# Kernel tuning notes

Hardware: AMD Instinct MI355X
Metric: run time of the kernel (lower is better)

The kernel has to match this reference:

```python
import math
import jax, jax.numpy as jnp
import numpy as np

N = 8192
D_IN = 512
D_E = 512


def setup_inputs() -> dict:
    key = jax.random.key(0)
    k1, k2, k3, k4 = jax.random.split(key, 4)
    x = jax.random.normal(k1, (N, D_IN), dtype=jnp.float32)
    A = jax.random.uniform(k2, (N, N), dtype=jnp.float32)
    # xavier-uniform-ish scaling for the two projection weights
    lim_qkv = math.sqrt(6.0 / (D_IN + 3 * D_E))
    Wqkv = jax.random.uniform(k3, (D_IN, 3 * D_E), dtype=jnp.float32, minval=-lim_qkv, maxval=lim_qkv)
    bqkv = jnp.zeros((3 * D_E,), dtype=jnp.float32)
    lim_o = math.sqrt(6.0 / (D_E + D_E))
    Wo = jax.random.uniform(k4, (D_E, D_E), dtype=jnp.float32, minval=-lim_o, maxval=lim_o)
    bo = jnp.zeros((D_E,), dtype=jnp.float32)
    return {"x": x, "A": A, "Wqkv": Wqkv, "bqkv": bqkv, "Wo": Wo, "bo": bo}


def reference(x, A, Wqkv, bqkv, Wo, bo):
    # qkv projection: [N, 3*D_E]
    qkv = x @ Wqkv + bqkv
    q, k, v = jnp.split(qkv, 3, axis=-1)  # each [N, D_E]
    # graph-adjacency transform of keys
    k = A @ k  # [N, D_E]
    scale = 1.0 / math.sqrt(q.shape[-1])
    attn_logits = (q @ k.T) * scale  # [N, N]
    attention = jax.nn.softmax(attn_logits, axis=-1)
    values = attention @ v  # [N, D_E]
    o = values @ Wo + bo
    return (o, attention)
```

## Files before the change

### kernel.cpp

```cpp
#include <hip/hip_runtime.h>

typedef _Float16 half8 __attribute__((ext_vector_type(8)));
typedef _Float16 half4 __attribute__((ext_vector_type(4)));
typedef float f32x4 __attribute__((ext_vector_type(4)));

__global__ __launch_bounds__(256) void transpose_f32(
    const float* __restrict__ in, int lda,
    float* __restrict__ out, int ldo)
{
  __shared__ float t[32][33];
  const int tx = threadIdx.x & 31, ty = threadIdx.x >> 5;
  const int bc = blockIdx.x * 32, br = blockIdx.y * 32;
#pragma unroll
  for (int i = 0; i < 4; ++i)
    t[ty + 8 * i][tx] = in[(size_t)(br + ty + 8 * i) * lda + bc + tx];
  __syncthreads();
#pragma unroll
  for (int i = 0; i < 4; ++i)
    out[(size_t)(bc + ty + 8 * i) * ldo + br + tx] = t[tx][ty + 8 * i];
}

__global__ __launch_bounds__(256) void transpose_f32_f16(
    const float* __restrict__ in, int lda,
    _Float16* __restrict__ out, int ldo)
{
  __shared__ float t[32][33];
  const int tx = threadIdx.x & 31, ty = threadIdx.x >> 5;
  const int bc = blockIdx.x * 32, br = blockIdx.y * 32;
#pragma unroll
  for (int i = 0; i < 4; ++i)
    t[ty + 8 * i][tx] = in[(size_t)(br + ty + 8 * i) * lda + bc + tx];
  __syncthreads();
#pragma unroll
  for (int i = 0; i < 4; ++i)
    out[(size_t)(bc + ty + 8 * i) * ldo + br + tx] = (_Float16)t[tx][ty + 8 * i];
}

__global__ __launch_bounds__(256) void transpose_f16(
    const _Float16* __restrict__ in, int lda,
    _Float16* __restrict__ out, int ldo)
{
  __shared__ _Float16 t[64][66];
  const int tx = threadIdx.x & 63, ty = threadIdx.x >> 6;
  const int bc = blockIdx.x * 64, br = blockIdx.y * 64;
#pragma unroll
  for (int i = 0; i < 16; ++i)
    t[ty + 4 * i][tx] = in[(size_t)(br + ty + 4 * i) * lda + bc + tx];
  __syncthreads();
#pragma unroll
  for (int i = 0; i < 16; ++i)
    out[(size_t)(bc + ty + 4 * i) * ldo + br + tx] = t[tx][ty + 4 * i];
}

__global__ __launch_bounds__(256) void conv_f32_f16(
    const float4* __restrict__ in, _Float16* __restrict__ out)
{
  size_t i = (size_t)blockIdx.x * 256 + threadIdx.x;
  float4 v = in[i];
  half4 h;
  h[0] = (_Float16)v.x; h[1] = (_Float16)v.y;
  h[2] = (_Float16)v.z; h[3] = (_Float16)v.w;
  ((half4*)out)[i] = h;
}

__global__ __launch_bounds__(256) void halfcolsum16(
    const _Float16* __restrict__ k0T16, float* __restrict__ csum)
{
  const int d = blockIdx.x, tid = threadIdx.x;
  float s = 0.f;
#pragma unroll
  for (int i = 0; i < 4; ++i) {
    half8 h = *(const half8*)(k0T16 + (size_t)d * 8192 + i * 2048 + tid * 8);
#pragma unroll
    for (int j = 0; j < 8; ++j) s += (float)h[j];
  }
#pragma unroll
  for (int off = 32; off; off >>= 1) s += __shfl_xor(s, off);
  __shared__ float r[4];
  if ((tid & 63) == 0) r[tid >> 6] = s;
  __syncthreads();
  if (tid == 0) csum[d] = 0.5f * ((r[0] + r[1]) + (r[2] + r[3]));
}

template<int ASPL,int BSPL,int BM,int BN,int WAVES_M,int WAVES_N,int THREADS,
         int APART,bool KSPLIT,int CMODE,int MINW,int AMODE,int BMODE>
__global__ __launch_bounds__(THREADS, MINW) void gemm_bt(
    const void* __restrict__ Agv, int lda, size_t a_plane,
    const void* __restrict__ Bgv, int ldb, size_t b_plane,
    float* __restrict__ Cg, int ldc, size_t c_plane,
    const float* __restrict__ bias, int K, float scale,
    _Float16* __restrict__ c16out)
{
  constexpr int BK = 32;
  constexpr int WM = BM / WAVES_M, WN = BN / WAVES_N;
  constexpr int FM = WM / 16, FN = WN / 16;
  constexpr int NCA = (BM * 4) / THREADS;
  constexpr int NCB = (BN * 4) / THREADS;
  static_assert((BM * 4) % THREADS == 0 && (BN * 4) % THREADS == 0, "mismatch");
  static_assert(AMODE != 3 || ASPL == 1, "AMODE 3 needs ASPL 1");

  __shared__ _Float16 ldsA[2][ASPL][BM][BK];
  __shared__ _Float16 ldsB[2][BSPL][BN][BK];

  const float*    Ag   = (const float*)Agv;
  const _Float16* Ag16 = (const _Float16*)Agv;
  const float*    Bg   = (const float*)Bgv;
  const _Float16* Bg16 = (const _Float16*)Bgv;

  const int tid  = threadIdx.x;
  const int lane = tid & 63;
  const int wid  = tid >> 6;
  const int wrow = wid / WAVES_N, wcol = wid % WAVES_N;
  const int l15  = lane & 15, g = lane >> 4;
  const int brow = blockIdx.y * BM;
  const int bcol = blockIdx.x * BN;

  if constexpr (KSPLIT) {
    const int kc = blockIdx.z;
    Ag += (size_t)kc * K;  Ag16 += (size_t)kc * K;
    Bg += (size_t)kc * K;  Bg16 += (size_t)kc * K;
    Cg += (size_t)kc * c_plane;
  }

  f32x4 acc[FM][FN];
#pragma unroll
  for (int mi = 0; mi < FM; ++mi)
#pragma unroll
    for (int ni = 0; ni < FN; ++ni)
      acc[mi][ni] = (f32x4){0.f, 0.f, 0.f, 0.f};

  float4 ra[NCA][2], rb[NCB][2];
  half8  rah[NCA], rbh[NCB];

  auto loadAB = [&](int kt) {
    const int k0 = kt * BK;
#pragma unroll
    for (int i = 0; i < NCA; ++i) {
      int c = tid + THREADS * i;
      int row = c >> 2, ci = c & 3;
      if constexpr (AMODE == 3) {
        rah[i] = *(const half8*)(Ag16 + (size_t)(brow + row) * lda + k0 + ci * 8);
      } else if constexpr (AMODE == 1) {
        float4 u0 = make_float4(0.f, 0.f, 0.f, 0.f);
        float4 u1 = make_float4(0.f, 0.f, 0.f, 0.f);
        const _Float16* bp = Ag16 + (size_t)(brow + row) * lda + k0 + ci * 8;
#pragma unroll
        for (int p = 0; p < APART; ++p) {
          half8 hv = *(const half8*)(bp + (size_t)p * a_plane);
          u0.x += (float)hv[0]; u0.y += (float)hv[1]; u0.z += (float)hv[2]; u0.w += (float)hv[3];
          u1.x += (float)hv[4]; u1.y += (float)hv[5]; u1.z += (float)hv[6]; u1.w += (float)hv[7];
        }
        ra[i][0] = u0; ra[i][1] = u1;
      } else {
        const float* bp = Ag + (size_t)(brow + row) * lda + k0 + ci * 8;
        float4 u0 = ((const float4*)bp)[0];
        float4 u1 = ((const float4*)bp)[1];
#pragma unroll
        for (int p = 1; p < APART; ++p) {
          const float* pp = bp + (size_t)p * a_plane;
          float4 w0 = ((const float4*)pp)[0], w1 = ((const float4*)pp)[1];
          u0.x += w0.x; u0.y += w0.y; u0.z += w0.z; u0.w += w0.w;
          u1.x += w1.x; u1.y += w1.y; u1.z += w1.z; u1.w += w1.w;
        }
        ra[i][0] = u0; ra[i][1] = u1;
      }
    }
#pragma unroll
    for (int i = 0; i < NCB; ++i) {
      int c = tid + THREADS * i;
      int row = c >> 2, ci = c & 3;
      if constexpr (BMODE == 3) {
        rbh[i] = *(const half8*)(Bg16 + (size_t)(bcol + row) * ldb + k0 + ci * 8);
      } else {
        const float4* p = (const float4*)(Bg + (size_t)(bcol + row) * ldb + k0 + ci * 8);
        rb[i][0] = p[0]; rb[i][1] = p[1];
      }
    }
  };

  auto stageLDS = [&](int b) {
#pragma unroll
    for (int i = 0; i < NCA; ++i) {
      int c = tid + THREADS * i;
      int row = c >> 2, ci = c & 3;
      int off = row * BK + ((ci ^ ((row >> 1) & 3)) << 3);
      if constexpr (AMODE == 3) {
        *(half8*)(&ldsA[b][0][0][0] + off) = rah[i];
      } else {
        float f[8] = {ra[i][0].x, ra[i][0].y, ra[i][0].z, ra[i][0].w,
                      ra[i][1].x, ra[i][1].y, ra[i][1].z, ra[i][1].w};
        half8 h, l;
#pragma unroll
        for (int j = 0; j < 8; ++j) {
          _Float16 hv = (_Float16)f[j];
          h[j] = hv;
          if (ASPL == 2) l[j] = (_Float16)(f[j] - (float)hv);
        }
        *(half8*)(&ldsA[b][0][0][0] + off) = h;
        if (ASPL == 2) *(half8*)(&ldsA[b][1][0][0] + off) = l;
      }
    }
#pragma unroll
    for (int i = 0; i < NCB; ++i) {
      int c = tid + THREADS * i;
      int row = c >> 2, ci = c & 3;
      int off = row * BK + ((ci ^ ((row >> 1) & 3)) << 3);
      if constexpr (BMODE == 3) {
        *(half8*)(&ldsB[b][0][0][0] + off) = rbh[i];
      } else {
        float f[8] = {rb[i][0].x, rb[i][0].y, rb[i][0].z, rb[i][0].w,
                      rb[i][1].x, rb[i][1].y, rb[i][1].z, rb[i][1].w};
        half8 h, l;
#pragma unroll
        for (int j = 0; j < 8; ++j) {
          _Float16 hv = (_Float16)f[j];
          h[j] = hv;
          if (BSPL == 2) l[j] = (_Float16)(f[j] - (float)hv);
        }
        *(half8*)(&ldsB[b][0][0][0] + off) = h;
        if (BSPL == 2) *(half8*)(&ldsB[b][1][0][0] + off) = l;
      }
    }
  };

  const int nk = K / BK;
  loadAB(0);
  stageLDS(0);
  if (nk > 1) loadAB(1);
  __syncthreads();

  for (int kt = 0; kt < nk; ++kt) {
    const int cur = kt & 1, nxt = cur ^ 1;
    if (kt + 1 < nk) stageLDS(nxt);
    if (kt + 2 < nk) loadAB(kt + 2);

    half8 af[FM][ASPL];
#pragma unroll
    for (int mi = 0; mi < FM; ++mi)
#pragma unroll
      for (int sa = 0; sa < ASPL; ++sa) {
        int row = wrow * WM + mi * 16 + l15;
        af[mi][sa] = *(const half8*)(&ldsA[cur][sa][0][0] + row * BK + ((g ^ ((row >> 1) & 3)) << 3));
      }
#pragma unroll
    for (int ni = 0; ni < FN; ++ni) {
      half8 bf[BSPL];
#pragma unroll
      for (int sb = 0; sb < BSPL; ++sb) {
        int row = wcol * WN + ni * 16 + l15;
        bf[sb] = *(const half8*)(&ldsB[cur][sb][0][0] + row * BK + ((g ^ ((row >> 1) & 3)) << 3));
      }
#pragma unroll
      for (int mi = 0; mi < FM; ++mi)
#pragma unroll
        for (int sa = 0; sa < ASPL; ++sa)
#pragma unroll
          for (int sb = 0; sb < BSPL; ++sb) {
            if (ASPL == 2 && BSPL == 2 && sa == 1 && sb == 1) continue;
            acc[mi][ni] = __builtin_amdgcn_mfma_f32_16x16x32_f16(af[mi][sa], bf[sb], acc[mi][ni], 0, 0, 0);
          }
    }
    __syncthreads();
  }

#pragma unroll
  for (int mi = 0; mi < FM; ++mi)
#pragma unroll
    for (int ni = 0; ni < FN; ++ni) {
      int col = bcol + wcol * WN + ni * 16 + l15;
      float bv = bias ? bias[col] : 0.f;
#pragma unroll
      for (int j = 0; j < 4; ++j) {
        int r = brow + wrow * WM + mi * 16 + g * 4 + j;
        float v = acc[mi][ni][j] * scale + bv;
        if constexpr (CMODE == 2) {
          c16out[(size_t)r * ldc + col] = (_Float16)v;
        } else {
          Cg[(size_t)r * ldc + col] = v;
        }
      }
    }
}

template<int BM,int BN,int THREADS,bool STATS,int MINW>
__global__ __launch_bounds__(THREADS, MINW) void gemm_ff16(
    const _Float16* __restrict__ Ag, int lda,
    const _Float16* __restrict__ Bg, int ldb,
    float* __restrict__ Cg, int ldc,
    int K, float scale,
    float* __restrict__ mxout, float* __restrict__ smout, int ntiles)
{
  constexpr int BK = 32;
  constexpr int WAVES_M = 2, WAVES_N = 2;
  constexpr int WM = BM / WAVES_M, WN = BN / WAVES_N;
  constexpr int FM = WM / 16, FN = WN / 16;
  constexpr int NCA = (BM * 4) / THREADS;
  constexpr int NCB = (BN * 4) / THREADS;

  __shared__ _Float16 ldsA[2][BM][BK];
  __shared__ _Float16 ldsB[2][BN][BK];

  const int tid  = threadIdx.x;
  const int lane = tid & 63;
  const int wid  = tid >> 6;
  const int wrow = wid >> 1, wcol = wid & 1;
  const int l15  = lane & 15, g = lane >> 4;

  const int id = blockIdx.x;
  const int wgid = (id & 7) * 512 + (id >> 3);
  const int bxv = wgid & 63, byv = wgid >> 6;
  const int brow = byv * BM;
  const int bcol = bxv * BN;

  f32x4 acc[FM][FN];
#pragma unroll
  for (int mi = 0; mi < FM; ++mi)
#pragma unroll
    for (int ni = 0; ni < FN; ++ni)
      acc[mi][ni] = (f32x4){0.f, 0.f, 0.f, 0.f};

  half8 ra[NCA], rb[NCB];

  auto loadAB = [&](int kt) {
    const int k0 = kt * BK;
#pragma unroll
    for (int i = 0; i < NCA; ++i) {
      int c = tid + THREADS * i;
      int row = c >> 2, ci = c & 3;
      ra[i] = *(const half8*)(Ag + (size_t)(brow + row) * lda + k0 + ci * 8);
    }
#pragma unroll
    for (int i = 0; i < NCB; ++i) {
      int c = tid + THREADS * i;
      int row = c >> 2, ci = c & 3;
      rb[i] = *(const half8*)(Bg + (size_t)(bcol + row) * ldb + k0 + ci * 8);
    }
  };

  auto stageLDS = [&](int b) {
#pragma unroll
    for (int i = 0; i < NCA; ++i) {
      int c = tid + THREADS * i;
      int row = c >> 2, ci = c & 3;
      int off = row * BK + ((ci ^ ((row >> 1) & 3)) << 3);
      *(half8*)(&ldsA[b][0][0] + off) = ra[i];
    }
#pragma unroll
    for (int i = 0; i < NCB; ++i) {
      int c = tid + THREADS * i;
      int row = c >> 2, ci = c & 3;
      int off = row * BK + ((ci ^ ((row >> 1) & 3)) << 3);
      *(half8*)(&ldsB[b][0][0] + off) = rb[i];
    }
  };

  const int nk = K / BK;
  loadAB(0);
  stageLDS(0);
  if (nk > 1) loadAB(1);
  __syncthreads();

  for (int kt = 0; kt < nk; ++kt) {
    const int cur = kt & 1, nxt = cur ^ 1;
    if (kt + 1 < nk) stageLDS(nxt);
    if (kt + 2 < nk) loadAB(kt + 2);

    half8 af[FM];
#pragma unroll
    for (int mi = 0; mi < FM; ++mi) {
      int row = wrow * WM + mi * 16 + l15;
      af[mi] = *(const half8*)(&ldsA[cur][0][0] + row * BK + ((g ^ ((row >> 1) & 3)) << 3));
    }
#pragma unroll
    for (int ni = 0; ni < FN; ++ni) {
      int row = wcol * WN + ni * 16 + l15;
      half8 bf = *(const half8*)(&ldsB[cur][0][0] + row * BK + ((g ^ ((row >> 1) & 3)) << 3));
#pragma unroll
      for (int mi = 0; mi < FM; ++mi)
        acc[mi][ni] = __builtin_amdgcn_mfma_f32_16x16x32_f16(af[mi], bf, acc[mi][ni], 0, 0, 0);
    }
    __syncthreads();
  }

#pragma unroll
  for (int mi = 0; mi < FM; ++mi)
#pragma unroll
    for (int ni = 0; ni < FN; ++ni) {
      int col = bcol + wcol * WN + ni * 16 + l15;
#pragma unroll
      for (int j = 0; j < 4; ++j) {
        int r = brow + wrow * WM + mi * 16 + g * 4 + j;
        Cg[(size_t)r * ldc + col] = acc[mi][ni][j] * scale;
      }
    }

  if constexpr (STATS) {
    __shared__ float s_m2[BM][2];
    __shared__ float s_s2[BM][2];
#pragma unroll
    for (int mi = 0; mi < FM; ++mi)
#pragma unroll
      for (int j = 0; j < 4; ++j) {
        float v = -3.4e38f;
#pragma unroll
        for (int ni = 0; ni < FN; ++ni) v = fmaxf(v, acc[mi][ni][j] * scale);
        v = fmaxf(v, __shfl_xor(v, 1)); v = fmaxf(v, __shfl_xor(v, 2));
        v = fmaxf(v, __shfl_xor(v, 4)); v = fmaxf(v, __shfl_xor(v, 8));
        if (l15 == 0) s_m2[wrow * WM + mi * 16 + g * 4 + j][wcol] = v;
      }
    __syncthreads();
#pragma unroll
    for (int mi = 0; mi < FM; ++mi)
#pragma unroll
      for (int j = 0; j < 4; ++j) {
        int r = wrow * WM + mi * 16 + g * 4 + j;
        float mt = fmaxf(s_m2[r][0], s_m2[r][1]);
        float s = 0.f;
#pragma unroll
        for (int ni = 0; ni < FN; ++ni) s += __expf(acc[mi][ni][j] * scale - mt);
        s += __shfl_xor(s, 1); s += __shfl_xor(s, 2);
        s += __shfl_xor(s, 4); s += __shfl_xor(s, 8);
        if (l15 == 0) s_s2[r][wcol] = s;
      }
    __syncthreads();
    if (tid < BM) {
      float mt = fmaxf(s_m2[tid][0], s_m2[tid][1]);
      float st = s_s2[tid][0] + s_s2[tid][1];
      mxout[(size_t)(brow + tid) * ntiles + bxv] = mt;
      smout[(size_t)(brow + tid) * ntiles + bxv] = st;
    }
  }
}

__global__ __launch_bounds__(256) void reduce4_f16(
    const float4* __restrict__ in, _Float16* __restrict__ out16, size_t plane4,
    const float4* __restrict__ csum4)
{
  size_t i = (size_t)blockIdx.x * 256 + threadIdx.x;
  float4 a = in[i], b = in[plane4 + i], c = in[2 * plane4 + i], d = in[3 * plane4 + i];
  float4 s = csum4[i & 127];
  half4 h;
  h[0] = (_Float16)(a.x + b.x + c.x + d.x - s.x);
  h[1] = (_Float16)(a.y + b.y + c.y + d.y - s.y);
  h[2] = (_Float16)(a.z + b.z + c.z + d.z - s.z);
  h[3] = (_Float16)(a.w + b.w + c.w + d.w - s.w);
  *(half4*)(out16 + i * 4) = h;
}

__global__ __launch_bounds__(256) void softmax_combine(
    const float* __restrict__ mx, const float* __restrict__ sm,
    float* __restrict__ rowm, float* __restrict__ rowinv)
{
  const int row = blockIdx.x * 4 + (threadIdx.x >> 6);
  const int lane = threadIdx.x & 63;
  float mt = mx[(size_t)row * 64 + lane];
  float m = mt;
#pragma unroll
  for (int off = 32; off; off >>= 1) m = fmaxf(m, __shfl_xor(m, off));
  float s = sm[(size_t)row * 64 + lane] * __expf(mt - m);
#pragma unroll
  for (int off = 32; off; off >>= 1) s += __shfl_xor(s, off);
  if (lane == 0) { rowm[row] = m; rowinv[row] = 1.0f / s; }
}

__global__ __launch_bounds__(512, 4) void pv_fused(
    float* __restrict__ attn,
    const _Float16* __restrict__ vT16,
    const float* __restrict__ rowm, const float* __restrict__ rowinv,
    _Float16* __restrict__ vals16)
{
  constexpr int BM = 64, BN = 512, BK = 32, NSTEP = 64;
  __shared__ _Float16 ldsA[2][BM][BK];
  __shared__ _Float16 ldsB[2][BN][BK];
  __shared__ float s_m[BM], s_inv[BM];

  const int tid = threadIdx.x, lane = tid & 63, wid = tid >> 6;
  const int wrow = wid >> 2, wcol = wid & 3;
  const int l15 = lane & 15, g = lane >> 4;
  const int kc = blockIdx.x, brow = blockIdx.y * BM;
  const size_t kbase = (size_t)kc * 2048;

  if (tid < BM) { s_m[tid] = rowm[brow + tid]; s_inv[tid] = rowinv[brow + tid]; }

  f32x4 acc[2][8];
#pragma unroll
  for (int mi = 0; mi < 2; ++mi)
#pragma unroll
    for (int ni = 0; ni < 8; ++ni) acc[mi][ni] = (f32x4){0.f, 0.f, 0.f, 0.f};

  const int arow = (tid & 255) >> 2, aci = tid & 3;
  float4 ra[2];
  half8 rbh[4];

  auto loadA = [&](int kt) {
    if (tid < 256) {
      const float4* p = (const float4*)(attn + (size_t)(brow + arow) * 8192 + kbase + kt * BK + aci * 8);
      ra[0] = p[0]; ra[1] = p[1];
    }
  };
  auto loadB = [&](int kt) {
#pragma unroll
    for (int i = 0; i < 4; ++i) {
      int c = tid + 512 * i; int r = c >> 2, ci = c & 3;
      rbh[i] = *(const half8*)(vT16 + (size_t)r * 8192 + kbase + kt * BK + ci * 8);
    }
  };
  auto stage = [&](int kt, int b) {
    if (tid < 256) {
      const float m = s_m[arow], inv = s_inv[arow];
      float f[8] = {ra[0].x, ra[0].y, ra[0].z, ra[0].w, ra[1].x, ra[1].y, ra[1].z, ra[1].w};
      float e[8]; half8 h;
#pragma unroll
      for (int j = 0; j < 8; ++j) {
        e[j] = __expf(f[j] - m) * inv;
        h[j] = (_Float16)e[j];
      }
      float4* w = (float4*)(attn + (size_t)(brow + arow) * 8192 + kbase + kt * BK + aci * 8);
      w[0] = make_float4(e[0], e[1], e[2], e[3]);
      w[1] = make_float4(e[4], e[5], e[6], e[7]);
      int off = arow * BK + ((aci ^ ((arow >> 1) & 3)) << 3);
      *(half8*)(&ldsA[b][0][0] + off) = h;
    }
#pragma unroll
    for (int i = 0; i < 4; ++i) {
      int c = tid + 512 * i; int r = c >> 2, ci = c & 3;
      int off2 = r * BK + ((ci ^ ((r >> 1) & 3)) << 3);
      *(half8*)(&ldsB[b][0][0] + off2) = rbh[i];
    }
  };

  loadA(0); loadB(0);
  __syncthreads();
  stage(0, 0);
  loadA(1); loadB(1);
  __syncthreads();

  for (int kt = 0; kt < NSTEP; ++kt) {
    const int cur = kt & 1, nxt = cur ^ 1;
    if (kt + 1 < NSTEP) stage(kt + 1, nxt);
    if (kt + 2 < NSTEP) { loadA(kt + 2); loadB(kt + 2); }
    half8 af[2];
#pragma unroll
    for (int mi = 0; mi < 2; ++mi) {
      int row = wrow * 32 + mi * 16 + l15;
      af[mi] = *(const half8*)(&ldsA[cur][0][0] + row * BK + ((g ^ ((row >> 1) & 3)) << 3));
    }
    __builtin_amdgcn_s_setprio(1);
#pragma unroll
    for (int ni = 0; ni < 8; ++ni) {
      int rn = wcol * 128 + ni * 16 + l15;
      half8 bf = *(const half8*)(&ldsB[cur][0][0] + rn * BK + ((g ^ ((rn >> 1) & 3)) << 3));
#pragma unroll
      for (int mi = 0; mi < 2; ++mi)
        acc[mi][ni] = __builtin_amdgcn_mfma_f32_16x16x32_f16(af[mi], bf, acc[mi][ni], 0, 0, 0);
    }
    __builtin_amdgcn_s_setprio(0);
    __syncthreads();
  }

  const size_t plane = (size_t)8192 * 512;
#pragma unroll
  for (int mi = 0; mi < 2; ++mi)
#pragma unroll
    for (int ni = 0; ni < 8; ++ni) {
      int col = wcol * 128 + ni * 16 + l15;
#pragma unroll
      for (int j = 0; j < 4; ++j) {
        int row = brow + wrow * 32 + mi * 16 + g * 4 + j;
        vals16[(size_t)kc * plane + (size_t)row * 512 + col] = (_Float16)acc[mi][ni][j];
      }
    }
}

extern "C" void kernel_launch(void* const* d_in, const int* in_sizes, int n_in,
                              void* d_out, int out_size, void* d_ws, size_t ws_size,
                              hipStream_t stream)
{
  const float* x    = (const float*)d_in[0];
  const float* Amat = (const float*)d_in[1];
  const float* Wqkv = (const float*)d_in[2];
  const float* bqkv = (const float*)d_in[3];
  const float* Wo   = (const float*)d_in[4];
  const float* bo   = (const float*)d_in[5];

  float* o    = (float*)d_out;
  float* attn = (float*)d_out + (size_t)8192 * 512;

  float* ws = (float*)d_ws;
  _Float16*  vals16 = (_Float16*)ws;
  _Float16*  qkv16  = (_Float16*)(ws + 8388608);
  _Float16*  k0T16  = (_Float16*)(ws + 14680064);
  _Float16*  vT16   = (_Float16*)(ws + 16777216);
  _Float16*  W16T   = (_Float16*)(ws + 18874368);
  float*     WoT    = ws + 19660800;
  _Float16*  kbuf16 = (_Float16*)(ws + 19922944);
  float*     mx     = ws + 24117248;
  float*     sm     = ws + 24641536;
  float*     rowm   = ws + 25165824;
  float*     rowinv = ws + 25174016;
  float*     csum   = ws + 25182208;
  float*     kpart  = attn;
  _Float16*  x16    = (_Float16*)attn;

  const dim3 b256(256), b512(512);
  const float qk_scale = 0.04419417382415922f;
  const size_t plane = (size_t)8192 * 512;

  conv_f32_f16<<<dim3(4096), b256, 0, stream>>>((const float4*)x, x16);
  transpose_f32_f16<<<dim3(48, 16), b256, 0, stream>>>(Wqkv, 1536, W16T, 512);
  transpose_f32<<<dim3(16, 16), b256, 0, stream>>>(Wo, 512, WoT, 512);

  gemm_bt<1, 1, 128, 128, 2, 2, 256, 1, false, 2, 4, 3, 3>
      <<<dim3(12, 64), b256, 0, stream>>>(
      x16, 512, 0, W16T, 512, 0, nullptr, 1536, 0, bqkv, 512, 1.0f, qkv16);

  transpose_f16<<<dim3(8, 128), b256, 0, stream>>>(qkv16 + 512, 1536, k0T16, 8192);
  transpose_f16<<<dim3(8, 128), b256, 0, stream>>>(qkv16 + 1024, 1536, vT16, 8192);
  halfcolsum16<<<dim3(512), b256, 0, stream>>>(k0T16, csum);

  gemm_bt<1, 1, 128, 256, 2, 4, 512, 1, true, 0, 4, 0, 3>
      <<<dim3(2, 64, 4), b512, 0, stream>>>(
      Amat, 8192, 0, k0T16, 8192, 0, kpart, 512, plane, nullptr, 2048, 1.0f, nullptr);

  reduce4_f16<<<dim3(4096), b256, 0, stream>>>((const float4*)kpart, kbuf16, plane / 4,
                                               (const float4*)csum);

  gemm_ff16<128, 128, 256, true, 4>
      <<<dim3(4096), b256, 0, stream>>>(
      qkv16, 1536, kbuf16, 512, attn, 8192, 512, qk_scale, mx, sm, 64);

  softmax_combine<<<dim3(2048), b256, 0, stream>>>(mx, sm, rowm, rowinv);

  pv_fused<<<dim3(4, 128), b512, 0, stream>>>(attn, vT16, rowm, rowinv, vals16);

  gemm_bt<1, 1, 128, 128, 2, 2, 256, 4, false, 0, 3, 1, 0>
      <<<dim3(4, 64), b256, 0, stream>>>(
      vals16, 512, plane, WoT, 512, 0, o, 512, 0, bo, 512, 1.0f, nullptr);
}
```

Baseline: 580.9 us.

## Store tile-max-shifted logits as fp16 intermediate instead of fp32 attention buffer

The QK^T kernel now writes logits minus their per-tile max as fp16 into a separate workspace buffer rather than fp32 into the attention output. The fused softmax-PV kernel reads these fp16 values and re-adds the tile max, which halves the intermediate read/write traffic over the N×N matrix. The cost is fp16 rounding of the shifted logits, which can reduce attention precision. The original fp32 path is kept as a fallback for when the workspace is too small.

```diff
diff --git a/kernel.cpp b/kernel.cpp
--- a/kernel.cpp
+++ b/kernel.cpp
@@ -282,11 +282,11 @@
     }
 }
 
-template<int BM,int BN,int THREADS,bool STATS,int MINW>
+template<int BM,int BN,int THREADS,bool STATS,int MINW,int CM>
 __global__ __launch_bounds__(THREADS, MINW) void gemm_ff16(
     const _Float16* __restrict__ Ag, int lda,
     const _Float16* __restrict__ Bg, int ldb,
-    float* __restrict__ Cg, int ldc,
+    float* __restrict__ Cg, _Float16* __restrict__ Cg16, int ldc,
     int K, float scale,
     float* __restrict__ mxout, float* __restrict__ smout, int ntiles)
 {
@@ -382,17 +382,19 @@
     __syncthreads();
   }
 
-#pragma unroll
-  for (int mi = 0; mi < FM; ++mi)
-#pragma unroll
-    for (int ni = 0; ni < FN; ++ni) {
-      int col = bcol + wcol * WN + ni * 16 + l15;
-#pragma unroll
-      for (int j = 0; j < 4; ++j) {
-        int r = brow + wrow * WM + mi * 16 + g * 4 + j;
-        Cg[(size_t)r * ldc + col] = acc[mi][ni][j] * scale;
-      }
-    }
+  if constexpr (CM == 0) {
+#pragma unroll
+    for (int mi = 0; mi < FM; ++mi)
+#pragma unroll
+      for (int ni = 0; ni < FN; ++ni) {
+        int col = bcol + wcol * WN + ni * 16 + l15;
+#pragma unroll
+        for (int j = 0; j < 4; ++j) {
+          int r = brow + wrow * WM + mi * 16 + g * 4 + j;
+          Cg[(size_t)r * ldc + col] = acc[mi][ni][j] * scale;
+        }
+      }
+  }
 
   if constexpr (STATS) {
     __shared__ float s_m2[BM][2];
@@ -417,7 +419,14 @@
         float mt = fmaxf(s_m2[r][0], s_m2[r][1]);
         float s = 0.f;
 #pragma unroll
-        for (int ni = 0; ni < FN; ++ni) s += __expf(acc[mi][ni][j] * scale - mt);
+        for (int ni = 0; ni < FN; ++ni) {
+          float lv = acc[mi][ni][j] * scale - mt;
+          s += __expf(lv);
+          if constexpr (CM == 1) {
+            int col = bcol + wcol * WN + ni * 16 + l15;
+            Cg16[(size_t)(brow + r) * ldc + col] = (_Float16)lv;
+          }
+        }
         s += __shfl_xor(s, 1); s += __shfl_xor(s, 2);
         s += __shfl_xor(s, 4); s += __shfl_xor(s, 8);
         if (l15 == 0) s_s2[r][wcol] = s;
@@ -463,16 +472,20 @@
   if (lane == 0) { rowm[row] = m; rowinv[row] = 1.0f / s; }
 }
 
+template<int A16>
 __global__ __launch_bounds__(512, 4) void pv_fused(
-    float* __restrict__ attn,
+    const void* __restrict__ lin,
+    float* __restrict__ attn_out,
     const _Float16* __restrict__ vT16,
     const float* __restrict__ rowm, const float* __restrict__ rowinv,
+    const float* __restrict__ mxbuf,
     _Float16* __restrict__ vals16)
 {
   constexpr int BM = 64, BN = 512, BK = 32, NSTEP = 64;
   __shared__ _Float16 ldsA[2][BM][BK];
   __shared__ _Float16 ldsB[2][BN][BK];
   __shared__ float s_m[BM], s_inv[BM];
+  __shared__ float s_mt[BM][16];
 
   const int tid = threadIdx.x, lane = tid & 63, wid = tid >> 6;
   const int wrow = wid >> 2, wcol = wid & 3;
@@ -480,7 +493,18 @@
   const int kc = blockIdx.x, brow = blockIdx.y * BM;
   const size_t kbase = (size_t)kc * 2048;
 
+  const float*    lf32 = (const float*)lin;
+  const _Float16* lf16 = (const _Float16*)lin;
+
   if (tid < BM) { s_m[tid] = rowm[brow + tid]; s_inv[tid] = rowinv[brow + tid]; }
+  if constexpr (A16 == 1) {
+#pragma unroll
+    for (int i = 0; i < 2; ++i) {
+      int idx = tid + i * 512;
+      int row = idx >> 4, t = idx & 15;
+      s_mt[row][t] = mxbuf[(size_t)(brow + row) * 64 + kc * 16 + t];
+    }
+  }
 
   f32x4 acc[2][8];
 #pragma unroll
@@ -490,12 +514,17 @@
 
   const int arow = (tid & 255) >> 2, aci = tid & 3;
   float4 ra[2];
+  half8 ra16;
   half8 rbh[4];
 
   auto loadA = [&](int kt) {
     if (tid < 256) {
-      const float4* p = (const float4*)(attn + (size_t)(brow + arow) * 8192 + kbase + kt * BK + aci * 8);
-      ra[0] = p[0]; ra[1] = p[1];
+      if constexpr (A16 == 1) {
+        ra16 = *(const half8*)(lf16 + (size_t)(brow + arow) * 8192 + kbase + kt * BK + aci * 8);
+      } else {
+        const float4* p = (const float4*)(lf32 + (size_t)(brow + arow) * 8192 + kbase + kt * BK + aci * 8);
+        ra[0] = p[0]; ra[1] = p[1];
+      }
     }
   };
   auto loadB = [&](int kt) {
@@ -508,14 +537,23 @@
   auto stage = [&](int kt, int b) {
     if (tid < 256) {
       const float m = s_m[arow], inv = s_inv[arow];
-      float f[8] = {ra[0].x, ra[0].y, ra[0].z, ra[0].w, ra[1].x, ra[1].y, ra[1].z, ra[1].w};
+      float f[8];
+      float madj;
+      if constexpr (A16 == 1) {
+        madj = s_mt[arow][kt >> 2] - m;
+#pragma unroll
+        for (int j = 0; j < 8; ++j) f[j] = (float)ra16[j] + madj;
+      } else {
+#pragma unroll
+        for (int j = 0; j < 4; ++j) { f[j] = (&ra[0].x)[j] - m; f[4 + j] = (&ra[1].x)[j] - m; }
+      }
       float e[8]; half8 h;
 #pragma unroll
       for (int j = 0; j < 8; ++j) {
-        e[j] = __expf(f[j] - m) * inv;
+        e[j] = __expf(f[j]) * inv;
         h[j] = (_Float16)e[j];
       }
-      float4* w = (float4*)(attn + (size_t)(brow + arow) * 8192 + kbase + kt * BK + aci * 8);
+      float4* w = (float4*)(attn_out + (size_t)(brow + arow) * 8192 + kbase + kt * BK + aci * 8);
       w[0] = make_float4(e[0], e[1], e[2], e[3]);
       w[1] = make_float4(e[4], e[5], e[6], e[7]);
       int off = arow * BK + ((aci ^ ((arow >> 1) & 3)) << 3);
@@ -599,8 +637,11 @@
   float*     rowm   = ws + 25165824;
   float*     rowinv = ws + 25174016;
   float*     csum   = ws + 25182208;
+  _Float16*  attn16 = (_Float16*)(ws + 25184256);
   float*     kpart  = attn;
   _Float16*  x16    = (_Float16*)attn;
+
+  const bool bigws = ws_size >= (size_t)(25184256 + 33554432) * 4;
 
   const dim3 b256(256), b512(512);
   const float qk_scale = 0.04419417382415922f;
@@ -625,13 +666,21 @@
   reduce4_f16<<<dim3(4096), b256, 0, stream>>>((const float4*)kpart, kbuf16, plane / 4,
                                                (const float4*)csum);
 
-  gemm_ff16<128, 128, 256, true, 4>
-      <<<dim3(4096), b256, 0, stream>>>(
-      qkv16, 1536, kbuf16, 512, attn, 8192, 512, qk_scale, mx, sm, 64);
-
-  softmax_combine<<<dim3(2048), b256, 0, stream>>>(mx, sm, rowm, rowinv);
-
-  pv_fused<<<dim3(4, 128), b512, 0, stream>>>(attn, vT16, rowm, rowinv, vals16);
+  if (bigws) {
+    gemm_ff16<128, 128, 256, true, 4, 1>
+        <<<dim3(4096), b256, 0, stream>>>(
+        qkv16, 1536, kbuf16, 512, nullptr, attn16, 8192, 512, qk_scale, mx, sm, 64);
+    softmax_combine<<<dim3(2048), b256, 0, stream>>>(mx, sm, rowm, rowinv);
+    pv_fused<1><<<dim3(4, 128), b512, 0, stream>>>(
+        attn16, attn, vT16, rowm, rowinv, mx, vals16);
+  } else {
+    gemm_ff16<128, 128, 256, true, 4, 0>
+        <<<dim3(4096), b256, 0, stream>>>(
+        qkv16, 1536, kbuf16, 512, attn, nullptr, 8192, 512, qk_scale, mx, sm, 64);
+    softmax_combine<<<dim3(2048), b256, 0, stream>>>(mx, sm, rowm, rowinv);
+    pv_fused<0><<<dim3(4, 128), b512, 0, stream>>>(
+        attn, attn, vT16, rowm, rowinv, nullptr, vals16);
+  }
 
   gemm_bt<1, 1, 128, 128, 2, 2, 256, 4, false, 0, 3, 1, 0>
       <<<dim3(4, 64), b256, 0, stream>>>(
```

Measured after the change: 547.3 us. 1.06x faster.
